# Optimization experiments

Measured on AMD Instinct MI355X. Metric: run time of the kernel, lower is better.

## Reference

```python
import jax, jax.numpy as jnp
import numpy as np
from jax import lax

N = 100000   # n_nodes
E = 600000   # n_edges (no self loops by construction)
D = 128      # hidden_dim
L = 3        # n_hops
K = 5        # tail_k_threshold


def setup_inputs() -> dict:
    key = jax.random.key(0)
    ks = jax.random.split(key, 10)
    x = jax.random.normal(ks[0], (N, D), dtype=jnp.float32)
    src = jax.random.randint(ks[1], (E,), 0, N)
    off = jax.random.randint(ks[2], (E,), 1, N)
    dst = (src + off) % N  # guarantees dst != src (self loops removed in original)
    s = 1.0 / np.sqrt(D)
    def U(k, shape):
        return jax.random.uniform(k, shape, minval=-s, maxval=s, dtype=jnp.float32)
    return {
        "x": x,
        "G1": U(ks[3], (L, D, D)), "G2": U(ks[4], (L, D, D)),
        "B1": U(ks[5], (L, D, D)), "B2": U(ks[6], (L, D, D)),
        "R": U(ks[7], (L, D)),
        "edge_src": src, "edge_dst": dst,
    }


def _lrelu(v):
    return jax.nn.leaky_relu(v, 0.2)


def reference(x, G1, G2, B1, B2, R, edge_src, edge_dst):
    # row degrees of adj (A[src, dst] = 1)
    deg = jax.ops.segment_sum(jnp.ones(E, jnp.float32), edge_src, num_segments=N)
    inv_d = jnp.where(deg > 0, 1.0 / jnp.maximum(deg, 1.0), 0.0)   # left norm D^-1 A
    inv_d1 = 1.0 / (deg + 1.0)                                      # (A+I) left norm
    inv_d2 = 1.0 / (deg + 2.0)                                      # +1 virtual node
    w0, w1, w2 = inv_d[edge_src], inv_d1[edge_src], inv_d2[edge_src]
    head_mask = deg > K

    def spmm(w_edge, h):  # (D^-1 A) @ h via gather-scale-scatter
        return jax.ops.segment_sum(w_edge[:, None] * h[edge_dst], edge_src, num_segments=N)

    def propagate(head):
        h = x
        embs = [h]
        sups = []
        for l in range(L):
            nb = spmm(w0, h)
            ft = lax.stop_gradient(h)
            nbd = lax.stop_gradient(nb)
            gamma = _lrelu(ft @ G1[l].T + nbd @ G2[l].T) + 1.0
            beta = _lrelu(ft @ B1[l].T + nbd @ B2[l].T)
            m = ft + gamma * R[l] + beta - nbd   # missing_info (Relation, ablation=0)
            sups.append(m)
            if head:
                h = spmm(w1, h) + inv_d1[:, None] * h
            else:
                h = spmm(w2, h) + inv_d2[:, None] * h + m * inv_d2[:, None]
            embs.append(h)
        emb = jnp.mean(jnp.stack(embs, 0), 0)
        sup = jnp.mean(jnp.stack(sups, 0), 0)
        return emb, sup

    emb_h, _ = propagate(True)
    emb_t, _ = propagate(False)
    node_emb = jnp.where(head_mask[:, None], emb_h, emb_t)
    return node_emb
```

## Files before the change

### kernel.cpp

```cpp
#include <hip/hip_runtime.h>

#define N_NODES 100000
#define N_EDGES 600000
#define DIM 128
#define SCAN_B 1024
#define NCHUNK 98

typedef __attribute__((ext_vector_type(4))) float f32x4;
typedef __attribute__((ext_vector_type(8))) short bf16x8;
typedef __attribute__((ext_vector_type(4))) unsigned short u16x4;
typedef __attribute__((ext_vector_type(8))) unsigned short u16x8;

__device__ __forceinline__ unsigned short f2bf(float f) {
    union { float f; unsigned u; } cv; cv.f = f;
    unsigned r = (cv.u + 0x7FFFu + ((cv.u >> 16) & 1u)) >> 16;
    return (unsigned short)r;
}
__device__ __forceinline__ float bf2f(unsigned short v) {
    union { unsigned u; float f; } c; c.u = ((unsigned)v) << 16; return c.f;
}


__global__ void k_degree(const int* __restrict__ src, int* __restrict__ degi) {
    int e = blockIdx.x * 256 + threadIdx.x;
    if (e < N_EDGES) atomicAdd(&degi[src[e]], 1);
}

__global__ void k_chunksum(const int* __restrict__ degi, int* __restrict__ bsum) {
    __shared__ int sm[SCAN_B];
    int i = blockIdx.x * SCAN_B + threadIdx.x;
    sm[threadIdx.x] = (i < N_NODES) ? degi[i] : 0;
    __syncthreads();
    for (int s = SCAN_B / 2; s > 0; s >>= 1) {
        if (threadIdx.x < (unsigned)s) sm[threadIdx.x] += sm[threadIdx.x + s];
        __syncthreads();
    }
    if (threadIdx.x == 0) bsum[blockIdx.x] = sm[0];
}

__global__ void k_scanb(int* __restrict__ bsum, int nb) {
    __shared__ int sm[128];
    int t = threadIdx.x;
    int v = (t < nb) ? bsum[t] : 0;
    sm[t] = v; __syncthreads();
    for (int s = 1; s < 128; s <<= 1) {
        int a = (t >= s) ? sm[t - s] : 0;
        __syncthreads();
        sm[t] += a;
        __syncthreads();
    }
    if (t < nb) bsum[t] = sm[t] - v;
}

__global__ void k_rowptr(const int* __restrict__ degi, const int* __restrict__ bsum,
                         int* __restrict__ rowptr, int* __restrict__ cnt,
                         float* __restrict__ inv0, float* __restrict__ inv1,
                         float* __restrict__ inv2) {
    __shared__ int sm[SCAN_B];
    int i = blockIdx.x * SCAN_B + threadIdx.x;
    int v = (i < N_NODES) ? degi[i] : 0;
    sm[threadIdx.x] = v; __syncthreads();
    for (int s = 1; s < SCAN_B; s <<= 1) {
        int a = (threadIdx.x >= (unsigned)s) ? sm[threadIdx.x - s] : 0;
        __syncthreads();
        sm[threadIdx.x] += a;
        __syncthreads();
    }
    if (i < N_NODES) {
        int excl = bsum[blockIdx.x] + sm[threadIdx.x] - v;
        rowptr[i] = excl;
        cnt[i] = excl;
        float d = (float)v;
        inv0[i] = (v > 0) ? 1.0f / d : 0.0f;
        inv1[i] = 1.0f / (d + 1.0f);
        inv2[i] = 1.0f / (d + 2.0f);
    }
}

__global__ void k_fill(const int* __restrict__ src, const int* __restrict__ dst,
                       int* __restrict__ cnt, int* __restrict__ col) {
    int e = blockIdx.x * 256 + threadIdx.x;
    if (e < N_EDGES) {
        int pos = atomicAdd(&cnt[src[e]], 1);
        col[pos] = dst[e];
    }
}

__global__ void k_pack(const float* __restrict__ G1, const float* __restrict__ G2,
                       const float* __restrict__ B1, const float* __restrict__ B2,
                       short* __restrict__ Wp) {
    int idx = blockIdx.x * 256 + threadIdx.x;
    int j = idx & 7, lane = (idx >> 3) & 63, nt = (idx >> 9) & 15, kb = (idx >> 13) & 7, l = idx >> 16;
    int k = kb * 32 + (lane >> 4) * 8 + j;
    int n = nt * 16 + (lane & 15);
    float v;
    if (n < 128) {
        v = (k < 128) ? G1[(l * 128 + n) * 128 + k] : G2[(l * 128 + n) * 128 + (k - 128)];
    } else {
        int n2 = n - 128;
        v = (k < 128) ? B1[(l * 128 + n2) * 128 + k] : B2[(l * 128 + n2) * 128 + (k - 128)];
    }
    Wp[idx] = (short)f2bf(v);
}

__global__ void k_xcast(const float* __restrict__ x, unsigned short* __restrict__ xb) {
    int i = (blockIdx.x * 256 + threadIdx.x) * 4;
    f32x4 v = *(const f32x4*)(x + i);
    unsigned short o0 = f2bf(v[0]), o1 = f2bf(v[1]), o2 = f2bf(v[2]), o3 = f2bf(v[3]);
    unsigned long long pk = (unsigned long long)o0 | ((unsigned long long)o1 << 16)
                          | ((unsigned long long)o2 << 32) | ((unsigned long long)o3 << 48);
    *(unsigned long long*)(xb + i) = pk;
}


__device__ __forceinline__ void gather4(const u16x8* __restrict__ h8,
        const int* __restrict__ col, int start, int d, int lane, float* acc) {
    int c = lane & 15;
    int base = lane & 48;
    int dd = d < 16 ? d : 16;
    int idx = (c < dd) ? col[start + c] : 0;
    int dm = d;
    int tmx = __shfl_xor(dm, 16);
    dm = dm > tmx ? dm : tmx;
    tmx = __shfl_xor(dm, 32);
    dm = dm > tmx ? dm : tmx;
    int dmain = dm < 16 ? dm : 16;
    int e = 0;
    for (; e + 2 <= dmain; e += 2) {
        int c0 = __shfl(idx, base + e, 64);
        int c1 = __shfl(idx, base + e + 1, 64);
        if (e < d) {
            u16x8 v = h8[(size_t)c0 * 16 + c];
#pragma unroll
            for (int j = 0; j < 8; ++j) acc[j] += bf2f(v[j]);
        }
        if (e + 1 < d) {
            u16x8 v = h8[(size_t)c1 * 16 + c];
#pragma unroll
            for (int j = 0; j < 8; ++j) acc[j] += bf2f(v[j]);
        }
    }
    if (e < dmain) {
        int c0 = __shfl(idx, base + e, 64);
        if (e < d) {
            u16x8 v = h8[(size_t)c0 * 16 + c];
#pragma unroll
            for (int j = 0; j < 8; ++j) acc[j] += bf2f(v[j]);
        }
        ++e;
    }
    if (dm > 16) {
        for (; e < d; ++e) {
            int c0 = col[start + e];
            u16x8 v = h8[(size_t)c0 * 16 + c];
#pragma unroll
            for (int j = 0; j < 8; ++j) acc[j] += bf2f(v[j]);
        }
    }
}

__global__ __launch_bounds__(256) void k_agg0(
    const unsigned short* __restrict__ xb, unsigned short* __restrict__ Sb,
    unsigned short* __restrict__ hA, const float* __restrict__ inv1,
    const int* __restrict__ rowptr, const int* __restrict__ degi,
    const int* __restrict__ col)
{
    int lane = threadIdx.x & 63;
    int wid = (blockIdx.x * 256 + threadIdx.x) >> 6;
    int g = lane >> 4, c = lane & 15;
    int row = wid * 4 + g;
    int start = rowptr[row], d = degi[row];
    float acc[8] = {0,0,0,0,0,0,0,0};
    gather4((const u16x8*)xb, col, start, d, lane, acc);
    u16x8 hv = ((const u16x8*)xb)[(size_t)row * 16 + c];
    float w = inv1[row];
    u16x8 so, ho;
#pragma unroll
    for (int j = 0; j < 8; ++j) {
        so[j] = f2bf(acc[j]);
        ho[j] = f2bf(w * (acc[j] + bf2f(hv[j])));
    }
    ((u16x8*)Sb)[(size_t)row * 16 + c] = so;
    ((u16x8*)hA)[(size_t)row * 16 + c] = ho;
}

__global__ __launch_bounds__(256) void k_agg_head4(
    const unsigned short* __restrict__ hsrc, unsigned short* __restrict__ hnext,
    const unsigned short* __restrict__ xb, const unsigned short* __restrict__ h1b,
    float* __restrict__ outp, const float* __restrict__ inv1,
    const int* __restrict__ rowptr, const int* __restrict__ degi,
    const int* __restrict__ col, int final_hop)
{
    int lane = threadIdx.x & 63;
    int wid = (blockIdx.x * 256 + threadIdx.x) >> 6;
    int g = lane >> 4, c = lane & 15;
    int row = wid * 4 + g;
    int start = rowptr[row], d = degi[row];
    float acc[8] = {0,0,0,0,0,0,0,0};
    gather4((const u16x8*)hsrc, col, start, d, lane, acc);
    u16x8 hv = ((const u16x8*)hsrc)[(size_t)row * 16 + c];
    float w = inv1[row];
    float hn[8];
#pragma unroll
    for (int j = 0; j < 8; ++j) hn[j] = w * (acc[j] + bf2f(hv[j]));
    if (!final_hop) {
        u16x8 ho;
#pragma unroll
        for (int j = 0; j < 8; ++j) ho[j] = f2bf(hn[j]);
        ((u16x8*)hnext)[(size_t)row * 16 + c] = ho;
    } else {
        u16x8 xv = ((const u16x8*)xb)[(size_t)row * 16 + c];
        u16x8 h1 = ((const u16x8*)h1b)[(size_t)row * 16 + c];
        f32x4 e0, e1;
#pragma unroll
        for (int j = 0; j < 4; ++j)
            e0[j] = 0.25f * (bf2f(xv[j]) + bf2f(h1[j]) + bf2f(hv[j]) + hn[j]);
#pragma unroll
        for (int j = 0; j < 4; ++j)
            e1[j] = 0.25f * (bf2f(xv[4 + j]) + bf2f(h1[4 + j]) + bf2f(hv[4 + j]) + hn[4 + j]);
        float* op = outp + (size_t)row * DIM + c * 8;
        *(f32x4*)op = e0;
        *(f32x4*)(op + 4) = e1;
    }
}

__global__ __launch_bounds__(256) void k_agg_tail4(
    const unsigned short* __restrict__ hsrc, unsigned short* __restrict__ Sb,
    const int* __restrict__ rowptr, const int* __restrict__ degi,
    const int* __restrict__ col)
{
    int lane = threadIdx.x & 63;
    int wid = (blockIdx.x * 256 + threadIdx.x) >> 6;
    int g = lane >> 4, c = lane & 15;
    int row = wid * 4 + g;
    int start = rowptr[row], d = degi[row];
    float acc[8] = {0,0,0,0,0,0,0,0};
    gather4((const u16x8*)hsrc, col, start, d, lane, acc);
    u16x8 so;
#pragma unroll
    for (int j = 0; j < 8; ++j) so[j] = f2bf(acc[j]);
    ((u16x8*)Sb)[(size_t)row * 16 + c] = so;
}

__global__ __launch_bounds__(256) void k_gemm_tail(
    const unsigned short* __restrict__ hb, const unsigned short* __restrict__ Sb,
    unsigned short* __restrict__ hb_next,
    const unsigned short* __restrict__ xb, const unsigned short* __restrict__ h1b,
    float* __restrict__ outp,
    const float* __restrict__ Rl, const short* __restrict__ Wp,
    const float* __restrict__ inv0, const float* __restrict__ inv2,
    const int* __restrict__ degi, int last)
{
    __shared__ __align__(16) char smraw[33792];
    short* smW = (short*)smraw;
    float (*zb)[8][264] = (float(*)[8][264])smraw;

    int wave = threadIdx.x >> 6, lane = threadIdx.x & 63;
    int quad = lane >> 4, m16 = lane & 15;
    int r0 = blockIdx.x * 64 + wave * 16;
    int rowA = r0 + m16;
    int cA = rowA < N_NODES ? rowA : N_NODES - 1;
    float w0 = inv0[cA];
    const unsigned short* hrow = hb + (size_t)cA * DIM;
    const unsigned short* srow = Sb + (size_t)cA * DIM;

    f32x4 acc[16];
    const f32x4 vz = {0.f, 0.f, 0.f, 0.f};
#pragma unroll
    for (int t = 0; t < 16; ++t) acc[t] = vz;

    {
        const int4* g = (const int4*)Wp;
        int4* sd = (int4*)smW;
#pragma unroll
        for (int j = 0; j < 4; ++j) sd[j * 256 + threadIdx.x] = g[j * 256 + threadIdx.x];
    }

#pragma unroll
    for (int kb = 0; kb < 8; ++kb) {
        bf16x8 a;
        if (kb < 4) {
            a = *(const bf16x8*)(hrow + kb * 32 + quad * 8);
        } else {
            u16x8 sv = *(const u16x8*)(srow + (kb - 4) * 32 + quad * 8);
#pragma unroll
            for (int j = 0; j < 8; ++j) a[j] = (short)f2bf(w0 * bf2f(sv[j]));
        }
        __syncthreads();
        if (kb < 7) {
            const int4* g = (const int4*)(Wp + (kb + 1) * 8192);
            int4* sd = (int4*)(smW + ((kb + 1) & 1) * 8192);
#pragma unroll
            for (int j = 0; j < 4; ++j) sd[j * 256 + threadIdx.x] = g[j * 256 + threadIdx.x];
        }
        const short* wb = smW + (kb & 1) * 8192 + lane * 8;
#pragma unroll
        for (int nt = 0; nt < 16; ++nt) {
            bf16x8 b = *(const bf16x8*)(wb + nt * 512);
            acc[nt] = __builtin_amdgcn_mfma_f32_16x16x32_bf16(a, b, acc[nt], 0, 0, 0);
        }
    }
    __syncthreads();

    int c4 = (lane & 31) * 4;
    int halfsel = lane >> 5;
    f32x4 Rv = *(const f32x4*)(Rl + c4);

#pragma unroll
    for (int s = 0; s < 2; ++s) {
        if ((quad >> 1) == s) {
            int lr = (quad & 1) * 4;
#pragma unroll
            for (int nt = 0; nt < 16; ++nt)
#pragma unroll
                for (int r = 0; r < 4; ++r)
                    zb[wave][lr + r][nt * 16 + m16] = acc[nt][r];
        }
        __syncthreads();
#pragma unroll
        for (int it = 0; it < 4; ++it) {
            int lr = it * 2 + halfsel;
            int gi = r0 + s * 8 + lr;
            if (gi < N_NODES) {
                f32x4 z1 = *(const f32x4*)&zb[wave][lr][c4];
                f32x4 z2 = *(const f32x4*)&zb[wave][lr][128 + c4];
                u16x4 hu = *(const u16x4*)(hb + (size_t)gi * DIM + c4);
                u16x4 su = *(const u16x4*)(Sb + (size_t)gi * DIM + c4);
                float wi0 = inv0[gi], wi2 = inv2[gi];
                f32x4 hn, hvf;
#pragma unroll
                for (int j = 0; j < 4; ++j) {
                    float h = bf2f(hu[j]);
                    float sva = bf2f(su[j]);
                    float nb = wi0 * sva;
                    float g = (z1[j] > 0.f ? z1[j] : 0.2f * z1[j]) + 1.0f;
                    float be = (z2[j] > 0.f ? z2[j] : 0.2f * z2[j]);
                    float mm = h + g * Rv[j] + be - nb;
                    hn[j] = wi2 * (sva + h + mm);
                    hvf[j] = h;
                }
                if (!last) {
                    u16x4 o;
#pragma unroll
                    for (int j = 0; j < 4; ++j) o[j] = f2bf(hn[j]);
                    *(u16x4*)(hb_next + (size_t)gi * DIM + c4) = o;
                } else if (degi[gi] <= 5) {
                    u16x4 xu  = *(const u16x4*)(xb  + (size_t)gi * DIM + c4);
                    u16x4 h1u = *(const u16x4*)(h1b + (size_t)gi * DIM + c4);
                    f32x4 ev;
#pragma unroll
                    for (int j = 0; j < 4; ++j)
                        ev[j] = 0.25f * (bf2f(xu[j]) + bf2f(h1u[j]) + hvf[j] + hn[j]);
                    *(f32x4*)(outp + (size_t)gi * DIM + c4) = ev;
                }
            }
        }
        __syncthreads();
    }
}


extern "C" void kernel_launch(void* const* d_in, const int* in_sizes, int n_in,
                              void* d_out, int out_size, void* d_ws, size_t ws_size,
                              hipStream_t stream) {
    const float* x  = (const float*)d_in[0];
    const float* G1 = (const float*)d_in[1];
    const float* G2 = (const float*)d_in[2];
    const float* B1 = (const float*)d_in[3];
    const float* B2 = (const float*)d_in[4];
    const float* R  = (const float*)d_in[5];
    const int* esrc = (const int*)d_in[6];
    const int* edst = (const int*)d_in[7];
    float* out = (float*)d_out;

    char* base = (char*)d_ws;
    size_t off = 0;
    auto alloc = [&](size_t b) -> void* {
        void* p = base + off;
        off = (off + b + 255) & ~(size_t)255;
        return p;
    };
    int* degi   = (int*)alloc(4 * N_NODES);
    int* rowptr = (int*)alloc(4 * N_NODES);
    int* cnt    = (int*)alloc(4 * N_NODES);
    int* bsum   = (int*)alloc(4 * 256);
    int* col    = (int*)alloc(4 * N_EDGES);
    float* inv0 = (float*)alloc(4 * N_NODES);
    float* inv1 = (float*)alloc(4 * N_NODES);
    float* inv2 = (float*)alloc(4 * N_NODES);
    short* Wp   = (short*)alloc(2 * 3 * 65536);
    unsigned short* xb = (unsigned short*)alloc(2ull * N_NODES * DIM);
    unsigned short* hA = (unsigned short*)alloc(2ull * N_NODES * DIM);
    unsigned short* hB = (unsigned short*)alloc(2ull * N_NODES * DIM);
    unsigned short* tA = (unsigned short*)alloc(2ull * N_NODES * DIM);
    unsigned short* Sb = (unsigned short*)alloc(2ull * N_NODES * DIM);

    hipMemsetAsync(degi, 0, 4 * N_NODES, stream);
    k_degree<<<(N_EDGES + 255) / 256, 256, 0, stream>>>(esrc, degi);
    k_chunksum<<<NCHUNK, SCAN_B, 0, stream>>>(degi, bsum);
    k_scanb<<<1, 128, 0, stream>>>(bsum, NCHUNK);
    k_rowptr<<<NCHUNK, SCAN_B, 0, stream>>>(degi, bsum, rowptr, cnt, inv0, inv1, inv2);
    k_fill<<<(N_EDGES + 255) / 256, 256, 0, stream>>>(esrc, edst, cnt, col);
    k_pack<<<768, 256, 0, stream>>>(G1, G2, B1, B2, Wp);
    k_xcast<<<12500, 256, 0, stream>>>(x, xb);

    k_agg0<<<6250, 256, 0, stream>>>(xb, Sb, hA, inv1, rowptr, degi, col);
    k_gemm_tail<<<1563, 256, 0, stream>>>(xb, Sb, tA, xb, tA, out, R, Wp, inv0, inv2, degi, 0);

    k_agg_head4<<<6250, 256, 0, stream>>>(hA, hB, xb, hA, out, inv1, rowptr, degi, col, 0);
    k_agg_head4<<<6250, 256, 0, stream>>>(hB, hB, xb, hA, out, inv1, rowptr, degi, col, 1);

    k_agg_tail4<<<6250, 256, 0, stream>>>(tA, Sb, rowptr, degi, col);
    k_gemm_tail<<<1563, 256, 0, stream>>>(tA, Sb, hB, xb, tA, out, R + 128, Wp + 65536, inv0, inv2, degi, 0);
    k_agg_tail4<<<6250, 256, 0, stream>>>(hB, Sb, rowptr, degi, col);
    k_gemm_tail<<<1563, 256, 0, stream>>>(hB, Sb, hB, xb, tA, out, R + 256, Wp + 131072, inv0, inv2, degi, 1);
}
```

Before: 481.4 us.

## Co-schedule independent head and tail hops in merged kernels, unroll gather by four

```diff
diff --git a/kernel.cpp b/kernel.cpp
--- a/kernel.cpp
+++ b/kernel.cpp
@@ -5,6 +5,8 @@
 #define DIM 128
 #define SCAN_B 1024
 #define NCHUNK 98
+#define GEMM_BLOCKS 1563
+#define AGG_BLOCKS 6250
 
 typedef __attribute__((ext_vector_type(4))) float f32x4;
 typedef __attribute__((ext_vector_type(8))) short bf16x8;
@@ -126,9 +128,11 @@
     dm = dm > tmx ? dm : tmx;
     int dmain = dm < 16 ? dm : 16;
     int e = 0;
-    for (; e + 2 <= dmain; e += 2) {
+    for (; e + 4 <= dmain; e += 4) {
         int c0 = __shfl(idx, base + e, 64);
         int c1 = __shfl(idx, base + e + 1, 64);
+        int c2 = __shfl(idx, base + e + 2, 64);
+        int c3 = __shfl(idx, base + e + 3, 64);
         if (e < d) {
             u16x8 v = h8[(size_t)c0 * 16 + c];
 #pragma unroll
@@ -139,15 +143,24 @@
 #pragma unroll
             for (int j = 0; j < 8; ++j) acc[j] += bf2f(v[j]);
         }
-    }
-    if (e < dmain) {
+        if (e + 2 < d) {
+            u16x8 v = h8[(size_t)c2 * 16 + c];
+#pragma unroll
+            for (int j = 0; j < 8; ++j) acc[j] += bf2f(v[j]);
+        }
+        if (e + 3 < d) {
+            u16x8 v = h8[(size_t)c3 * 16 + c];
+#pragma unroll
+            for (int j = 0; j < 8; ++j) acc[j] += bf2f(v[j]);
+        }
+    }
+    for (; e < dmain; ++e) {
         int c0 = __shfl(idx, base + e, 64);
         if (e < d) {
             u16x8 v = h8[(size_t)c0 * 16 + c];
 #pragma unroll
             for (int j = 0; j < 8; ++j) acc[j] += bf2f(v[j]);
         }
-        ++e;
     }
     if (dm > 16) {
         for (; e < d; ++e) {
@@ -159,47 +172,21 @@
     }
 }
 
-__global__ __launch_bounds__(256) void k_agg0(
-    const unsigned short* __restrict__ xb, unsigned short* __restrict__ Sb,
-    unsigned short* __restrict__ hA, const float* __restrict__ inv1,
-    const int* __restrict__ rowptr, const int* __restrict__ degi,
-    const int* __restrict__ col)
-{
-    int lane = threadIdx.x & 63;
-    int wid = (blockIdx.x * 256 + threadIdx.x) >> 6;
+
+__device__ __forceinline__ void agg_head_body(
+    int wid, const unsigned short* __restrict__ hsrc, unsigned short* __restrict__ hnext,
+    const unsigned short* __restrict__ xb, const unsigned short* __restrict__ h1b,
+    float* __restrict__ outp, const float* __restrict__ inv1,
+    const int* __restrict__ rowptr, const int* __restrict__ degi,
+    const int* __restrict__ col, int final_hop, int lane)
+{
     int g = lane >> 4, c = lane & 15;
     int row = wid * 4 + g;
     int start = rowptr[row], d = degi[row];
-    float acc[8] = {0,0,0,0,0,0,0,0};
-    gather4((const u16x8*)xb, col, start, d, lane, acc);
-    u16x8 hv = ((const u16x8*)xb)[(size_t)row * 16 + c];
+    u16x8 hv = ((const u16x8*)hsrc)[(size_t)row * 16 + c];
     float w = inv1[row];
-    u16x8 so, ho;
-#pragma unroll
-    for (int j = 0; j < 8; ++j) {
-        so[j] = f2bf(acc[j]);
-        ho[j] = f2bf(w * (acc[j] + bf2f(hv[j])));
-    }
-    ((u16x8*)Sb)[(size_t)row * 16 + c] = so;
-    ((u16x8*)hA)[(size_t)row * 16 + c] = ho;
-}
-
-__global__ __launch_bounds__(256) void k_agg_head4(
-    const unsigned short* __restrict__ hsrc, unsigned short* __restrict__ hnext,
-    const unsigned short* __restrict__ xb, const unsigned short* __restrict__ h1b,
-    float* __restrict__ outp, const float* __restrict__ inv1,
-    const int* __restrict__ rowptr, const int* __restrict__ degi,
-    const int* __restrict__ col, int final_hop)
-{
-    int lane = threadIdx.x & 63;
-    int wid = (blockIdx.x * 256 + threadIdx.x) >> 6;
-    int g = lane >> 4, c = lane & 15;
-    int row = wid * 4 + g;
-    int start = rowptr[row], d = degi[row];
     float acc[8] = {0,0,0,0,0,0,0,0};
     gather4((const u16x8*)hsrc, col, start, d, lane, acc);
-    u16x8 hv = ((const u16x8*)hsrc)[(size_t)row * 16 + c];
-    float w = inv1[row];
     float hn[8];
 #pragma unroll
     for (int j = 0; j < 8; ++j) hn[j] = w * (acc[j] + bf2f(hv[j]));
@@ -224,13 +211,11 @@
     }
 }
 
-__global__ __launch_bounds__(256) void k_agg_tail4(
-    const unsigned short* __restrict__ hsrc, unsigned short* __restrict__ Sb,
-    const int* __restrict__ rowptr, const int* __restrict__ degi,
-    const int* __restrict__ col)
-{
-    int lane = threadIdx.x & 63;
-    int wid = (blockIdx.x * 256 + threadIdx.x) >> 6;
+__device__ __forceinline__ void agg_tail_body(
+    int wid, const unsigned short* __restrict__ hsrc, unsigned short* __restrict__ Sb,
+    const int* __restrict__ rowptr, const int* __restrict__ degi,
+    const int* __restrict__ col, int lane)
+{
     int g = lane >> 4, c = lane & 15;
     int row = wid * 4 + g;
     int start = rowptr[row], d = degi[row];
@@ -242,22 +227,21 @@
     ((u16x8*)Sb)[(size_t)row * 16 + c] = so;
 }
 
-__global__ __launch_bounds__(256) void k_gemm_tail(
-    const unsigned short* __restrict__ hb, const unsigned short* __restrict__ Sb,
+__device__ __forceinline__ void gemm_tail_body(
+    int bx, const unsigned short* __restrict__ hb, const unsigned short* __restrict__ Sb,
     unsigned short* __restrict__ hb_next,
     const unsigned short* __restrict__ xb, const unsigned short* __restrict__ h1b,
     float* __restrict__ outp,
     const float* __restrict__ Rl, const short* __restrict__ Wp,
     const float* __restrict__ inv0, const float* __restrict__ inv2,
-    const int* __restrict__ degi, int last)
-{
-    __shared__ __align__(16) char smraw[33792];
+    const int* __restrict__ degi, int last, char* smraw)
+{
     short* smW = (short*)smraw;
     float (*zb)[8][264] = (float(*)[8][264])smraw;
 
     int wave = threadIdx.x >> 6, lane = threadIdx.x & 63;
     int quad = lane >> 4, m16 = lane & 15;
-    int r0 = blockIdx.x * 64 + wave * 16;
+    int r0 = bx * 64 + wave * 16;
     int rowA = r0 + m16;
     int cA = rowA < N_NODES ? rowA : N_NODES - 1;
     float w0 = inv0[cA];
@@ -357,6 +341,95 @@
         }
         __syncthreads();
     }
+}
+
+
+__global__ __launch_bounds__(256) void k_agg0(
+    const unsigned short* __restrict__ xb, unsigned short* __restrict__ Sb,
+    unsigned short* __restrict__ hA, const float* __restrict__ inv1,
+    const int* __restrict__ rowptr, const int* __restrict__ degi,
+    const int* __restrict__ col)
+{
+    int lane = threadIdx.x & 63;
+    int wid = (blockIdx.x * 256 + threadIdx.x) >> 6;
+    int g = lane >> 4, c = lane & 15;
+    int row = wid * 4 + g;
+    int start = rowptr[row], d = degi[row];
+    u16x8 hv = ((const u16x8*)xb)[(size_t)row * 16 + c];
+    float w = inv1[row];
+    float acc[8] = {0,0,0,0,0,0,0,0};
+    gather4((const u16x8*)xb, col, start, d, lane, acc);
+    u16x8 so, ho;
+#pragma unroll
+    for (int j = 0; j < 8; ++j) {
+        so[j] = f2bf(acc[j]);
+        ho[j] = f2bf(w * (acc[j] + bf2f(hv[j])));
+    }
+    ((u16x8*)Sb)[(size_t)row * 16 + c] = so;
+    ((u16x8*)hA)[(size_t)row * 16 + c] = ho;
+}
+
+__global__ __launch_bounds__(256) void k_hop1(
+    const unsigned short* __restrict__ xb, const unsigned short* __restrict__ Sb,
+    unsigned short* __restrict__ tA,
+    const unsigned short* __restrict__ hA, unsigned short* __restrict__ hC,
+    const float* __restrict__ Rl, const short* __restrict__ Wp,
+    const float* __restrict__ inv0, const float* __restrict__ inv1,
+    const float* __restrict__ inv2,
+    const int* __restrict__ rowptr, const int* __restrict__ degi,
+    const int* __restrict__ col)
+{
+    __shared__ __align__(16) char smraw[33792];
+    if (blockIdx.x < GEMM_BLOCKS) {
+        gemm_tail_body(blockIdx.x, xb, Sb, tA, xb, tA, (float*)nullptr,
+                       Rl, Wp, inv0, inv2, degi, 0, smraw);
+    } else {
+        int wid = ((blockIdx.x - GEMM_BLOCKS) * 256 + threadIdx.x) >> 6;
+        agg_head_body(wid, hA, hC, xb, hA, (float*)nullptr, inv1,
+                      rowptr, degi, col, 0, threadIdx.x & 63);
+    }
+}
+
+__global__ __launch_bounds__(256) void k_pair2(
+    const unsigned short* __restrict__ hC, const unsigned short* __restrict__ xb,
+    const unsigned short* __restrict__ hA, float* __restrict__ outp,
+    const unsigned short* __restrict__ tA, unsigned short* __restrict__ Sb,
+    const float* __restrict__ inv1,
+    const int* __restrict__ rowptr, const int* __restrict__ degi,
+    const int* __restrict__ col)
+{
+    int lane = threadIdx.x & 63;
+    if (blockIdx.x < AGG_BLOCKS) {
+        int wid = (blockIdx.x * 256 + threadIdx.x) >> 6;
+        agg_head_body(wid, hC, (unsigned short*)nullptr, xb, hA, outp, inv1,
+                      rowptr, degi, col, 1, lane);
+    } else {
+        int wid = ((blockIdx.x - AGG_BLOCKS) * 256 + threadIdx.x) >> 6;
+        agg_tail_body(wid, tA, Sb, rowptr, degi, col, lane);
+    }
+}
+
+__global__ __launch_bounds__(256) void k_agg_tail4(
+    const unsigned short* __restrict__ hsrc, unsigned short* __restrict__ Sb,
+    const int* __restrict__ rowptr, const int* __restrict__ degi,
+    const int* __restrict__ col)
+{
+    int wid = (blockIdx.x * 256 + threadIdx.x) >> 6;
+    agg_tail_body(wid, hsrc, Sb, rowptr, degi, col, threadIdx.x & 63);
+}
+
+__global__ __launch_bounds__(256) void k_gemm_tail(
+    const unsigned short* __restrict__ hb, const unsigned short* __restrict__ Sb,
+    unsigned short* __restrict__ hb_next,
+    const unsigned short* __restrict__ xb, const unsigned short* __restrict__ h1b,
+    float* __restrict__ outp,
+    const float* __restrict__ Rl, const short* __restrict__ Wp,
+    const float* __restrict__ inv0, const float* __restrict__ inv2,
+    const int* __restrict__ degi, int last)
+{
+    __shared__ __align__(16) char smraw[33792];
+    gemm_tail_body(blockIdx.x, hb, Sb, hb_next, xb, h1b, outp,
+                   Rl, Wp, inv0, inv2, degi, last, smraw);
 }
 
 
@@ -391,8 +464,9 @@
     short* Wp   = (short*)alloc(2 * 3 * 65536);
     unsigned short* xb = (unsigned short*)alloc(2ull * N_NODES * DIM);
     unsigned short* hA = (unsigned short*)alloc(2ull * N_NODES * DIM);
-    unsigned short* hB = (unsigned short*)alloc(2ull * N_NODES * DIM);
+    unsigned short* hC = (unsigned short*)alloc(2ull * N_NODES * DIM);
     unsigned short* tA = (unsigned short*)alloc(2ull * N_NODES * DIM);
+    unsigned short* tB = (unsigned short*)alloc(2ull * N_NODES * DIM);
     unsigned short* Sb = (unsigned short*)alloc(2ull * N_NODES * DIM);
 
     hipMemsetAsync(degi, 0, 4 * N_NODES, stream);
@@ -404,14 +478,15 @@
     k_pack<<<768, 256, 0, stream>>>(G1, G2, B1, B2, Wp);
     k_xcast<<<12500, 256, 0, stream>>>(x, xb);
 
-    k_agg0<<<6250, 256, 0, stream>>>(xb, Sb, hA, inv1, rowptr, degi, col);
-    k_gemm_tail<<<1563, 256, 0, stream>>>(xb, Sb, tA, xb, tA, out, R, Wp, inv0, inv2, degi, 0);
-
-    k_agg_head4<<<6250, 256, 0, stream>>>(hA, hB, xb, hA, out, inv1, rowptr, degi, col, 0);
-    k_agg_head4<<<6250, 256, 0, stream>>>(hB, hB, xb, hA, out, inv1, rowptr, degi, col, 1);
-
-    k_agg_tail4<<<6250, 256, 0, stream>>>(tA, Sb, rowptr, degi, col);
-    k_gemm_tail<<<1563, 256, 0, stream>>>(tA, Sb, hB, xb, tA, out, R + 128, Wp + 65536, inv0, inv2, degi, 0);
-    k_agg_tail4<<<6250, 256, 0, stream>>>(hB, Sb, rowptr, degi, col);
-    k_gemm_tail<<<1563, 256, 0, stream>>>(hB, Sb, hB, xb, tA, out, R + 256, Wp + 131072, inv0, inv2, degi, 1);
-}
+    k_agg0<<<AGG_BLOCKS, 256, 0, stream>>>(xb, Sb, hA, inv1, rowptr, degi, col);
+
+    k_hop1<<<GEMM_BLOCKS + AGG_BLOCKS, 256, 0, stream>>>(
+        xb, Sb, tA, hA, hC, R, Wp, inv0, inv1, inv2, rowptr, degi, col);
+
+    k_pair2<<<2 * AGG_BLOCKS, 256, 0, stream>>>(
+        hC, xb, hA, out, tA, Sb, inv1, rowptr, degi, col);
+
+    k_gemm_tail<<<GEMM_BLOCKS, 256, 0, stream>>>(tA, Sb, tB, xb, tA, out, R + 128, Wp + 65536, inv0, inv2, degi, 0);
+    k_agg_tail4<<<AGG_BLOCKS, 256, 0, stream>>>(tB, Sb, rowptr, degi, col);
+    k_gemm_tail<<<GEMM_BLOCKS, 256, 0, stream>>>(tB, Sb, tB, xb, tA, out, R + 256, Wp + 131072, inv0, inv2, degi, 1);
+}
```

New measurement: 502.7 us. 1.04x slower.

## Split tail GEMM by column halves, precompute scaled neighbor sums, unroll gather by four

Applied to the files above, without the earlier changes.

```diff
diff --git a/kernel.cpp b/kernel.cpp
--- a/kernel.cpp
+++ b/kernel.cpp
@@ -5,6 +5,8 @@
 #define DIM 128
 #define SCAN_B 1024
 #define NCHUNK 98
+#define GEMM_BLOCKS 1564
+#define AGG_BLOCKS 6250
 
 typedef __attribute__((ext_vector_type(4))) float f32x4;
 typedef __attribute__((ext_vector_type(8))) short bf16x8;
@@ -90,8 +92,15 @@
                        const float* __restrict__ B1, const float* __restrict__ B2,
                        short* __restrict__ Wp) {
     int idx = blockIdx.x * 256 + threadIdx.x;
-    int j = idx & 7, lane = (idx >> 3) & 63, nt = (idx >> 9) & 15, kb = (idx >> 13) & 7, l = idx >> 16;
-    int k = kb * 32 + (lane >> 4) * 8 + j;
+    int j = idx & 7;
+    int lane = (idx >> 3) & 63;
+    int ntp = (idx >> 9) & 7;
+    int kb4 = (idx >> 12) & 3;
+    int kh = (idx >> 14) & 1;
+    int cg = (idx >> 15) & 1;
+    int l = idx >> 16;
+    int k = (kh * 4 + kb4) * 32 + (lane >> 4) * 8 + j;
+    int nt = (ntp < 4) ? (cg * 4 + ntp) : (8 + cg * 4 + (ntp - 4));
     int n = nt * 16 + (lane & 15);
     float v;
     if (n < 128) {
@@ -126,9 +135,11 @@
     dm = dm > tmx ? dm : tmx;
     int dmain = dm < 16 ? dm : 16;
     int e = 0;
-    for (; e + 2 <= dmain; e += 2) {
+    for (; e + 4 <= dmain; e += 4) {
         int c0 = __shfl(idx, base + e, 64);
         int c1 = __shfl(idx, base + e + 1, 64);
+        int c2 = __shfl(idx, base + e + 2, 64);
+        int c3 = __shfl(idx, base + e + 3, 64);
         if (e < d) {
             u16x8 v = h8[(size_t)c0 * 16 + c];
 #pragma unroll
@@ -139,15 +150,24 @@
 #pragma unroll
             for (int j = 0; j < 8; ++j) acc[j] += bf2f(v[j]);
         }
-    }
-    if (e < dmain) {
+        if (e + 2 < d) {
+            u16x8 v = h8[(size_t)c2 * 16 + c];
+#pragma unroll
+            for (int j = 0; j < 8; ++j) acc[j] += bf2f(v[j]);
+        }
+        if (e + 3 < d) {
+            u16x8 v = h8[(size_t)c3 * 16 + c];
+#pragma unroll
+            for (int j = 0; j < 8; ++j) acc[j] += bf2f(v[j]);
+        }
+    }
+    for (; e < dmain; ++e) {
         int c0 = __shfl(idx, base + e, 64);
         if (e < d) {
             u16x8 v = h8[(size_t)c0 * 16 + c];
 #pragma unroll
             for (int j = 0; j < 8; ++j) acc[j] += bf2f(v[j]);
         }
-        ++e;
     }
     if (dm > 16) {
         for (; e < d; ++e) {
@@ -159,9 +179,11 @@
     }
 }
 
+
 __global__ __launch_bounds__(256) void k_agg0(
     const unsigned short* __restrict__ xb, unsigned short* __restrict__ Sb,
-    unsigned short* __restrict__ hA, const float* __restrict__ inv1,
+    unsigned short* __restrict__ Nb, unsigned short* __restrict__ hA,
+    const float* __restrict__ inv0, const float* __restrict__ inv1,
     const int* __restrict__ rowptr, const int* __restrict__ degi,
     const int* __restrict__ col)
 {
@@ -170,17 +192,19 @@
     int g = lane >> 4, c = lane & 15;
     int row = wid * 4 + g;
     int start = rowptr[row], d = degi[row];
+    u16x8 hv = ((const u16x8*)xb)[(size_t)row * 16 + c];
+    float w0 = inv0[row], w1 = inv1[row];
     float acc[8] = {0,0,0,0,0,0,0,0};
     gather4((const u16x8*)xb, col, start, d, lane, acc);
-    u16x8 hv = ((const u16x8*)xb)[(size_t)row * 16 + c];
-    float w = inv1[row];
-    u16x8 so, ho;
+    u16x8 so, no, ho;
 #pragma unroll
     for (int j = 0; j < 8; ++j) {
         so[j] = f2bf(acc[j]);
-        ho[j] = f2bf(w * (acc[j] + bf2f(hv[j])));
+        no[j] = f2bf(w0 * acc[j]);
+        ho[j] = f2bf(w1 * (acc[j] + bf2f(hv[j])));
     }
     ((u16x8*)Sb)[(size_t)row * 16 + c] = so;
+    ((u16x8*)Nb)[(size_t)row * 16 + c] = no;
     ((u16x8*)hA)[(size_t)row * 16 + c] = ho;
 }
 
@@ -196,10 +220,10 @@
     int g = lane >> 4, c = lane & 15;
     int row = wid * 4 + g;
     int start = rowptr[row], d = degi[row];
+    u16x8 hv = ((const u16x8*)hsrc)[(size_t)row * 16 + c];
+    float w = inv1[row];
     float acc[8] = {0,0,0,0,0,0,0,0};
     gather4((const u16x8*)hsrc, col, start, d, lane, acc);
-    u16x8 hv = ((const u16x8*)hsrc)[(size_t)row * 16 + c];
-    float w = inv1[row];
     float hn[8];
 #pragma unroll
     for (int j = 0; j < 8; ++j) hn[j] = w * (acc[j] + bf2f(hv[j]));
@@ -226,6 +250,7 @@
 
 __global__ __launch_bounds__(256) void k_agg_tail4(
     const unsigned short* __restrict__ hsrc, unsigned short* __restrict__ Sb,
+    unsigned short* __restrict__ Nb, const float* __restrict__ inv0,
     const int* __restrict__ rowptr, const int* __restrict__ degi,
     const int* __restrict__ col)
 {
@@ -234,18 +259,24 @@
     int g = lane >> 4, c = lane & 15;
     int row = wid * 4 + g;
     int start = rowptr[row], d = degi[row];
+    float w0 = inv0[row];
     float acc[8] = {0,0,0,0,0,0,0,0};
     gather4((const u16x8*)hsrc, col, start, d, lane, acc);
-    u16x8 so;
-#pragma unroll
-    for (int j = 0; j < 8; ++j) so[j] = f2bf(acc[j]);
+    u16x8 so, no;
+#pragma unroll
+    for (int j = 0; j < 8; ++j) {
+        so[j] = f2bf(acc[j]);
+        no[j] = f2bf(w0 * acc[j]);
+    }
     ((u16x8*)Sb)[(size_t)row * 16 + c] = so;
+    ((u16x8*)Nb)[(size_t)row * 16 + c] = no;
 }
 
 __global__ __launch_bounds__(256) void k_gemm_tail(
     const unsigned short* __restrict__ hb, const unsigned short* __restrict__ Sb,
+    const unsigned short* __restrict__ Nb,
     unsigned short* __restrict__ hb_next,
-    const unsigned short* __restrict__ xb, const unsigned short* __restrict__ h1b,
+    const unsigned short* __restrict__ xb, const unsigned short* __restrict__ t1b,
     float* __restrict__ outp,
     const float* __restrict__ Rl, const short* __restrict__ Wp,
     const float* __restrict__ inv0, const float* __restrict__ inv2,
@@ -253,79 +284,80 @@
 {
     __shared__ __align__(16) char smraw[33792];
     short* smW = (short*)smraw;
-    float (*zb)[8][264] = (float(*)[8][264])smraw;
 
     int wave = threadIdx.x >> 6, lane = threadIdx.x & 63;
     int quad = lane >> 4, m16 = lane & 15;
-    int r0 = blockIdx.x * 64 + wave * 16;
-    int rowA = r0 + m16;
-    int cA = rowA < N_NODES ? rowA : N_NODES - 1;
-    float w0 = inv0[cA];
-    const unsigned short* hrow = hb + (size_t)cA * DIM;
-    const unsigned short* srow = Sb + (size_t)cA * DIM;
-
-    f32x4 acc[16];
+    int cg = blockIdx.x & 1;
+    int rb = blockIdx.x >> 1;
+    int r0 = rb * 128 + wave * 32;
+
+    const unsigned short* arow[2][2];
+#pragma unroll
+    for (int rf = 0; rf < 2; ++rf) {
+        int rA = r0 + rf * 16 + m16;
+        int cA = rA < N_NODES ? rA : N_NODES - 1;
+        arow[0][rf] = hb + (size_t)cA * DIM;
+        arow[1][rf] = Nb + (size_t)cA * DIM;
+    }
+
+    f32x4 acc[2][8];
     const f32x4 vz = {0.f, 0.f, 0.f, 0.f};
 #pragma unroll
-    for (int t = 0; t < 16; ++t) acc[t] = vz;
-
-    {
-        const int4* g = (const int4*)Wp;
-        int4* sd = (int4*)smW;
-#pragma unroll
-        for (int j = 0; j < 4; ++j) sd[j * 256 + threadIdx.x] = g[j * 256 + threadIdx.x];
-    }
-
-#pragma unroll
-    for (int kb = 0; kb < 8; ++kb) {
-        bf16x8 a;
-        if (kb < 4) {
-            a = *(const bf16x8*)(hrow + kb * 32 + quad * 8);
-        } else {
-            u16x8 sv = *(const u16x8*)(srow + (kb - 4) * 32 + quad * 8);
-#pragma unroll
-            for (int j = 0; j < 8; ++j) a[j] = (short)f2bf(w0 * bf2f(sv[j]));
-        }
-        __syncthreads();
-        if (kb < 7) {
-            const int4* g = (const int4*)(Wp + (kb + 1) * 8192);
-            int4* sd = (int4*)(smW + ((kb + 1) & 1) * 8192);
-#pragma unroll
-            for (int j = 0; j < 4; ++j) sd[j * 256 + threadIdx.x] = g[j * 256 + threadIdx.x];
-        }
-        const short* wb = smW + (kb & 1) * 8192 + lane * 8;
-#pragma unroll
-        for (int nt = 0; nt < 16; ++nt) {
-            bf16x8 b = *(const bf16x8*)(wb + nt * 512);
-            acc[nt] = __builtin_amdgcn_mfma_f32_16x16x32_bf16(a, b, acc[nt], 0, 0, 0);
+    for (int rf = 0; rf < 2; ++rf)
+#pragma unroll
+        for (int t = 0; t < 8; ++t) acc[rf][t] = vz;
+
+#pragma unroll
+    for (int kh = 0; kh < 2; ++kh) {
+        if (kh) __syncthreads();
+        {
+            const int4* g = (const int4*)(Wp + (cg * 2 + kh) * 16384);
+            int4* sd = (int4*)smW;
+#pragma unroll
+            for (int jj = 0; jj < 8; ++jj)
+                sd[jj * 256 + threadIdx.x] = g[jj * 256 + threadIdx.x];
+        }
+        __syncthreads();
+#pragma unroll
+        for (int kb4 = 0; kb4 < 4; ++kb4) {
+            bf16x8 a0 = *(const bf16x8*)(arow[kh][0] + kb4 * 32 + quad * 8);
+            bf16x8 a1 = *(const bf16x8*)(arow[kh][1] + kb4 * 32 + quad * 8);
+            const short* wb = smW + kb4 * 4096 + lane * 8;
+#pragma unroll
+            for (int ntp = 0; ntp < 8; ++ntp) {
+                bf16x8 b = *(const bf16x8*)(wb + ntp * 512);
+                acc[0][ntp] = __builtin_amdgcn_mfma_f32_16x16x32_bf16(a0, b, acc[0][ntp], 0, 0, 0);
+                acc[1][ntp] = __builtin_amdgcn_mfma_f32_16x16x32_bf16(a1, b, acc[1][ntp], 0, 0, 0);
+            }
         }
     }
     __syncthreads();
 
-    int c4 = (lane & 31) * 4;
-    int halfsel = lane >> 5;
-    f32x4 Rv = *(const f32x4*)(Rl + c4);
-
-#pragma unroll
-    for (int s = 0; s < 2; ++s) {
-        if ((quad >> 1) == s) {
-            int lr = (quad & 1) * 4;
-#pragma unroll
-            for (int nt = 0; nt < 16; ++nt)
-#pragma unroll
-                for (int r = 0; r < 4; ++r)
-                    zb[wave][lr + r][nt * 16 + m16] = acc[nt][r];
-        }
-        __syncthreads();
-#pragma unroll
-        for (int it = 0; it < 4; ++it) {
-            int lr = it * 2 + halfsel;
-            int gi = r0 + s * 8 + lr;
+    float* zbw = (float*)smraw + wave * (16 * 132);
+    int cl = lane & 15, gg = lane >> 4;
+    int c4 = cl * 4;
+    int colbase = cg * 64;
+    f32x4 Rv = *(const f32x4*)(Rl + colbase + c4);
+
+#pragma unroll
+    for (int rf = 0; rf < 2; ++rf) {
+#pragma unroll
+        for (int ntp = 0; ntp < 8; ++ntp) {
+            int cofs = (ntp < 4) ? ntp * 16 : 64 + (ntp - 4) * 16;
+#pragma unroll
+            for (int r = 0; r < 4; ++r)
+                zbw[(quad * 4 + r) * 132 + cofs + m16] = acc[rf][ntp][r];
+        }
+#pragma unroll
+        for (int p = 0; p < 4; ++p) {
+            int lr = p * 4 + gg;
+            int gi = r0 + rf * 16 + lr;
             if (gi < N_NODES) {
-                f32x4 z1 = *(const f32x4*)&zb[wave][lr][c4];
-                f32x4 z2 = *(const f32x4*)&zb[wave][lr][128 + c4];
-                u16x4 hu = *(const u16x4*)(hb + (size_t)gi * DIM + c4);
-                u16x4 su = *(const u16x4*)(Sb + (size_t)gi * DIM + c4);
+                f32x4 z1 = *(const f32x4*)&zbw[lr * 132 + c4];
+                f32x4 z2 = *(const f32x4*)&zbw[lr * 132 + 64 + c4];
+                size_t o = (size_t)gi * DIM + colbase + c4;
+                u16x4 hu = *(const u16x4*)(hb + o);
+                u16x4 su = *(const u16x4*)(Sb + o);
                 float wi0 = inv0[gi], wi2 = inv2[gi];
                 f32x4 hn, hvf;
 #pragma unroll
@@ -340,22 +372,21 @@
                     hvf[j] = h;
                 }
                 if (!last) {
-                    u16x4 o;
-#pragma unroll
-                    for (int j = 0; j < 4; ++j) o[j] = f2bf(hn[j]);
-                    *(u16x4*)(hb_next + (size_t)gi * DIM + c4) = o;
+                    u16x4 ou;
+#pragma unroll
+                    for (int j = 0; j < 4; ++j) ou[j] = f2bf(hn[j]);
+                    *(u16x4*)(hb_next + o) = ou;
                 } else if (degi[gi] <= 5) {
-                    u16x4 xu  = *(const u16x4*)(xb  + (size_t)gi * DIM + c4);
-                    u16x4 h1u = *(const u16x4*)(h1b + (size_t)gi * DIM + c4);
+                    u16x4 xu  = *(const u16x4*)(xb  + o);
+                    u16x4 t1u = *(const u16x4*)(t1b + o);
                     f32x4 ev;
 #pragma unroll
                     for (int j = 0; j < 4; ++j)
-                        ev[j] = 0.25f * (bf2f(xu[j]) + bf2f(h1u[j]) + hvf[j] + hn[j]);
-                    *(f32x4*)(outp + (size_t)gi * DIM + c4) = ev;
+                        ev[j] = 0.25f * (bf2f(xu[j]) + bf2f(t1u[j]) + hvf[j] + hn[j]);
+                    *(f32x4*)(outp + o) = ev;
                 }
             }
         }
-        __syncthreads();
     }
 }
 
@@ -391,9 +422,11 @@
     short* Wp   = (short*)alloc(2 * 3 * 65536);
     unsigned short* xb = (unsigned short*)alloc(2ull * N_NODES * DIM);
     unsigned short* hA = (unsigned short*)alloc(2ull * N_NODES * DIM);
-    unsigned short* hB = (unsigned short*)alloc(2ull * N_NODES * DIM);
+    unsigned short* hC = (unsigned short*)alloc(2ull * N_NODES * DIM);
     unsigned short* tA = (unsigned short*)alloc(2ull * N_NODES * DIM);
     unsigned short* Sb = (unsigned short*)alloc(2ull * N_NODES * DIM);
+    unsigned short* Nb = (unsigned short*)alloc(2ull * N_NODES * DIM);
+    unsigned short* tB = hC;
 
     hipMemsetAsync(degi, 0, 4 * N_NODES, stream);
     k_degree<<<(N_EDGES + 255) / 256, 256, 0, stream>>>(esrc, degi);
@@ -404,14 +437,16 @@
     k_pack<<<768, 256, 0, stream>>>(G1, G2, B1, B2, Wp);
     k_xcast<<<12500, 256, 0, stream>>>(x, xb);
 
-    k_agg0<<<6250, 256, 0, stream>>>(xb, Sb, hA, inv1, rowptr, degi, col);
-    k_gemm_tail<<<1563, 256, 0, stream>>>(xb, Sb, tA, xb, tA, out, R, Wp, inv0, inv2, degi, 0);
-
-    k_agg_head4<<<6250, 256, 0, stream>>>(hA, hB, xb, hA, out, inv1, rowptr, degi, col, 0);
-    k_agg_head4<<<6250, 256, 0, stream>>>(hB, hB, xb, hA, out, inv1, rowptr, degi, col, 1);
-
-    k_agg_tail4<<<6250, 256, 0, stream>>>(tA, Sb, rowptr, degi, col);
-    k_gemm_tail<<<1563, 256, 0, stream>>>(tA, Sb, hB, xb, tA, out, R + 128, Wp + 65536, inv0, inv2, degi, 0);
-    k_agg_tail4<<<6250, 256, 0, stream>>>(hB, Sb, rowptr, degi, col);
-    k_gemm_tail<<<1563, 256, 0, stream>>>(hB, Sb, hB, xb, tA, out, R + 256, Wp + 131072, inv0, inv2, degi, 1);
-}
+    k_agg0<<<AGG_BLOCKS, 256, 0, stream>>>(xb, Sb, Nb, hA, inv0, inv1, rowptr, degi, col);
+
+    k_gemm_tail<<<GEMM_BLOCKS, 256, 0, stream>>>(xb, Sb, Nb, tA, xb, tA, out, R, Wp, inv0, inv2, degi, 0);
+
+    k_agg_head4<<<AGG_BLOCKS, 256, 0, stream>>>(hA, hC, xb, hA, out, inv1, rowptr, degi, col, 0);
+    k_agg_head4<<<AGG_BLOCKS, 256, 0, stream>>>(hC, hC, xb, hA, out, inv1, rowptr, degi, col, 1);
+
+    k_agg_tail4<<<AGG_BLOCKS, 256, 0, stream>>>(tA, Sb, Nb, inv0, rowptr, degi, col);
+    k_gemm_tail<<<GEMM_BLOCKS, 256, 0, stream>>>(tA, Sb, Nb, tB, xb, tA, out, R + 128, Wp + 65536, inv0, inv2, degi, 0);
+
+    k_agg_tail4<<<AGG_BLOCKS, 256, 0, stream>>>(tB, Sb, Nb, inv0, rowptr, degi, col);
+    k_gemm_tail<<<GEMM_BLOCKS, 256, 0, stream>>>(tB, Sb, Nb, tB, xb, tA, out, R + 256, Wp + 131072, inv0, inv2, degi, 1);
+}
```

After: 504.7 us. 4.8% more time.
